# Kernel tuning notes

Hardware: AMD Instinct MI355X
Metric: run time of the kernel (lower is better)

The kernel has to match this reference:

```python
import jax, jax.numpy as jnp
import numpy as np

B, S, F_IN = 64, 168, 10
D, H, L = 512, 8, 4
HID, F_OUT, N_FUT = 2048, 1, 48
EPS = 1e-9


def _pos_encoding(d, position=168):
    pos = np.arange(position)[:, None].astype(np.float32)
    i = np.arange(d)[None, :].astype(np.float32)
    angle = pos / np.power(10000.0, 2.0 * (np.floor(i / 2.0)) / np.float32(d))
    angle[:, 0::2] = np.sin(angle[:, 0::2])
    angle[:, 1::2] = np.cos(angle[:, 1::2])
    return jnp.asarray(angle[None, ...], dtype=jnp.float32)  # [1, position, d]


def setup_inputs() -> dict:
    key = jax.random.key(0)
    ks = iter(jax.random.split(key, 64))
    s = 0.02

    def w(shape):
        return (jax.random.normal(next(ks), shape, jnp.float32) * s)

    inp = {
        "x": jax.random.normal(next(ks), (B, S, F_IN), jnp.float32),
        "mask": jnp.triu(jnp.ones((S, S), jnp.float32), k=1)[None, None],  # [1,1,S,S]
        "in_w": w((F_IN, D)), "in_b": jnp.zeros((D,), jnp.float32),
        "wq_w": w((L, D, D * H)), "wq_b": jnp.zeros((L, D * H), jnp.float32),
        "wk_w": w((L, D, D * H)), "wk_b": jnp.zeros((L, D * H), jnp.float32),
        "wv_w": w((L, D, D * H)), "wv_b": jnp.zeros((L, D * H), jnp.float32),
        "dn_w": w((L, D * H, D)), "dn_b": jnp.zeros((L, D), jnp.float32),
        "mh_w": w((L, D, HID)), "mh_b": jnp.zeros((L, HID), jnp.float32),
        "mo_w": w((L, HID, D)), "mo_b": jnp.zeros((L, D), jnp.float32),
        "ln1_g": jnp.ones((L, D), jnp.float32), "ln1_b": jnp.zeros((L, D), jnp.float32),
        "ln3_g": jnp.ones((L, D), jnp.float32), "ln3_b": jnp.zeros((L, D), jnp.float32),
        "out_w": w((D, F_OUT)), "out_b": jnp.zeros((F_OUT,), jnp.float32),
    }
    return inp


def _ln(h, g, b):
    m = jnp.mean(h, axis=-1, keepdims=True)
    v = jnp.mean((h - m) ** 2, axis=-1, keepdims=True)
    return (h - m) * jax.lax.rsqrt(v + EPS) * g + b


def _split(t):  # [B,S,H*D] -> [B,H,S,D]
    return t.reshape(B, S, H, D).transpose(0, 2, 1, 3)


def reference(x, mask, in_w, in_b, wq_w, wq_b, wk_w, wk_b, wv_w, wv_b,
              dn_w, dn_b, mh_w, mh_b, mo_w, mo_b,
              ln1_g, ln1_b, ln3_g, ln3_b, out_w, out_b):
    pe = _pos_encoding(D)  # [1,168,D]
    h = x @ in_w + in_b
    h = h * jnp.sqrt(jnp.float32(D)) + pe[:, :S, :]
    inv_sqrt_d = 1.0 / jnp.sqrt(jnp.float32(D))
    for i in range(L):
        q = _split(h @ wq_w[i] + wq_b[i])
        k = _split(h @ wk_w[i] + wk_b[i])
        v = _split(h @ wv_w[i] + wv_b[i])
        scores = jnp.einsum('bhqd,bhkd->bhqk', q, k) * inv_sqrt_d
        scores = scores + mask * (-1e9)
        attn_w = jax.nn.softmax(scores, axis=-1)
        att = jnp.einsum('bhqk,bhkd->bhqd', attn_w, v)
        att = att.transpose(0, 2, 1, 3).reshape(B, S, H * D)
        att = att @ dn_w[i] + dn_b[i]
        h1 = _ln(att + h, ln1_g[i], ln1_b[i])
        mlp = jax.nn.relu(h1 @ mh_w[i] + mh_b[i]) @ mo_w[i] + mo_b[i]
        h = _ln(mlp + h1, ln3_g[i], ln3_b[i])
    out = h @ out_w + out_b
    return out[:, -N_FUT:, :]
```

## Files before the change

kernel.cpp:

```cpp
#include <hip/hip_runtime.h>
#include <hip/hip_bf16.h>

typedef __bf16 bf16;
typedef __bf16 bf16x8 __attribute__((ext_vector_type(8)));
typedef __bf16 bf16x4v __attribute__((ext_vector_type(4)));
typedef float f32x4 __attribute__((ext_vector_type(4)));

#define MODE_BIAS 1
#define MODE_RELU 2
#define MODE_BF16 4
#define MODE_F32  8
#define MODE_RES  16
#define MODE_RESB 32
#define MODE_QKV  128
#define MODE_ATOMIC 256

__device__ __forceinline__ void stage16(const bf16* g, bf16* l)
{
  __builtin_amdgcn_global_load_lds(
      (const __attribute__((address_space(1))) void*)g,
      (__attribute__((address_space(3))) void*)l, 16, 0, 0);
}

__global__ __launch_bounds__(256) void gemm2(
    const bf16* __restrict__ A, const bf16* __restrict__ B,
    float* __restrict__ Cf, bf16* __restrict__ Cb,
    const float* __restrict__ bias, const float* __restrict__ resf,
    const bf16* __restrict__ resb,
    int N, int K, int lda, int ldb, int ldc, long qstride, int mode)
{
  __shared__ __attribute__((aligned(16))) bf16 smem[16384];
  bf16* sA = smem;
  bf16* sB = smem + 8192;

  int tid  = threadIdx.x;
  int lane = tid & 63;
  int wave = tid >> 6;
  int wm = (wave >> 1) * 64;
  int wn = (wave & 1) * 64;

  int nwg = gridDim.x * gridDim.y;
  int i0  = blockIdx.y * gridDim.x + blockIdx.x;
  int q   = nwg >> 3, r = nwg & 7;
  int xcd = i0 & 7, jj = i0 >> 3;
  int lid = (xcd < r ? xcd * (q + 1) : r * (q + 1) + (xcd - r) * q) + jj;
  int bx = lid % gridDim.x;
  int by = lid / gridDim.x;
  int bm0 = bx * 128;
  int bn0 = by * 128;
  long ks = (long)blockIdx.z * K;

  f32x4 acc[4][4];
  #pragma unroll
  for (int i = 0; i < 4; ++i)
    #pragma unroll
    for (int j = 0; j < 4; ++j)
      #pragma unroll
      for (int rr = 0; rr < 4; ++rr) acc[i][j][rr] = 0.f;

  int seg0 = wave, seg1 = wave + 4;
  int csw = ((lane & 3) ^ ((lane >> 3) & 3)) * 16;
  int r0s = seg0 * 16 + (lane >> 2);
  int r1s = seg1 * 16 + (lane >> 2);
  int rx = ((lane >> 4) ^ ((lane >> 1) & 3)) * 8;

  const char* gA0 = (const char*)A + ((long)(bm0 + r0s) * lda + ks) * 2 + csw;
  const char* gA1 = (const char*)A + ((long)(bm0 + r1s) * lda + ks) * 2 + csw;
  const char* gB0 = (const char*)B + ((long)(bn0 + r0s) * ldb + ks) * 2 + csw;
  const char* gB1 = (const char*)B + ((long)(bn0 + r1s) * ldb + ks) * 2 + csw;

  int nt = K >> 5;

  stage16((const bf16*)gA0, sA + seg0 * 512);
  stage16((const bf16*)gA1, sA + seg1 * 512);
  stage16((const bf16*)gB0, sB + seg0 * 512);
  stage16((const bf16*)gB1, sB + seg1 * 512);

  for (int t = 0; t < nt; ++t) {
    int p = t & 1;
    if (t + 1 < nt) {
      long ob = (long)(t + 1) * 64;
      int so = (p ^ 1) * 4096;
      stage16((const bf16*)(gA0 + ob), sA + so + seg0 * 512);
      stage16((const bf16*)(gA1 + ob), sA + so + seg1 * 512);
      stage16((const bf16*)(gB0 + ob), sB + so + seg0 * 512);
      stage16((const bf16*)(gB1 + ob), sB + so + seg1 * 512);
      asm volatile("s_waitcnt vmcnt(4)" ::: "memory");
    } else {
      asm volatile("s_waitcnt vmcnt(0)" ::: "memory");
    }
    asm volatile("s_barrier" ::: "memory");
    __builtin_amdgcn_sched_barrier(0);
    int po = p * 4096;
    bf16x8 aF[4], bF[4];
    #pragma unroll
    for (int i = 0; i < 4; ++i)
      aF[i] = *(const bf16x8*)(&sA[po + (wm + i * 16 + (lane & 15)) * 32 + rx]);
    #pragma unroll
    for (int j = 0; j < 4; ++j)
      bF[j] = *(const bf16x8*)(&sB[po + (wn + j * 16 + (lane & 15)) * 32 + rx]);
    __builtin_amdgcn_s_setprio(1);
    #pragma unroll
    for (int i = 0; i < 4; ++i)
      #pragma unroll
      for (int j = 0; j < 4; ++j)
        acc[i][j] = __builtin_amdgcn_mfma_f32_16x16x32_bf16(aF[i], bF[j], acc[i][j], 0, 0, 0);
    __builtin_amdgcn_s_setprio(0);
    asm volatile("s_waitcnt lgkmcnt(0)" ::: "memory");
    __builtin_amdgcn_sched_barrier(0);
    asm volatile("s_barrier" ::: "memory");
  }

  int lg = lane >> 4;
  int r0 = lg * 4;
  int cc = lane & 15;

  if (mode & MODE_ATOMIC) {
    #pragma unroll
    for (int j = 0; j < 4; ++j) {
      int gn = bn0 + wn + j * 16 + cc;
      #pragma unroll
      for (int i = 0; i < 4; ++i)
        #pragma unroll
        for (int rr = 0; rr < 4; ++rr) {
          int gm = bm0 + wm + i * 16 + r0 + rr;
          unsafeAtomicAdd(&Cf[(long)gm * ldc + gn], acc[i][j][rr]);
        }
    }
    return;
  }

  if ((mode & MODE_QKV) && bn0 >= 8192) {
    bf16* sS = smem;
    int nn0 = bn0 - 8192;
    #pragma unroll
    for (int ph = 0; ph < 2; ++ph) {
      if ((wn >> 6) == ph) {
        #pragma unroll
        for (int j = 0; j < 4; ++j) {
          int nl = j * 16 + cc;
          float bv = bias[bn0 + wn + j * 16 + cc];
          #pragma unroll
          for (int i = 0; i < 4; ++i)
            #pragma unroll
            for (int rr = 0; rr < 4; ++rr) {
              int m = wm + i * 16 + r0 + rr;
              sS[nl * 130 + m] = (bf16)(acc[i][j][rr] + bv);
            }
        }
      }
      __syncthreads();
      #pragma unroll
      for (int u = 0; u < 16; ++u) {
        int nrow = u * 4 + wave;
        int d = nn0 + ph * 64 + nrow;
        int hh = d >> 9, dd = d & 511;
        unsigned int pv = *(const unsigned int*)&sS[nrow * 130 + lane * 2];
        int m0 = bm0 + 2 * lane;
        int bl = m0 / 168;
        int s  = m0 - bl * 168;
        *(unsigned int*)&Cb[2 * qstride + ((long)(bl * 8 + hh) * 512 + dd) * 168 + s] = pv;
      }
      __syncthreads();
    }
    return;
  }

  if (mode & (MODE_QKV | MODE_BF16)) {
    bf16* sS = smem;
    long base;
    int ldx;
    if (mode & MODE_QKV) {
      int part = bn0 >> 12;
      base = (long)part * qstride + (bn0 & 4095);
      ldx = 4096;
    } else {
      base = (long)bn0;
      ldx = ldc;
    }
    #pragma unroll
    for (int ph = 0; ph < 2; ++ph) {
      if ((wm >> 6) == ph) {
        #pragma unroll
        for (int j = 0; j < 4; ++j) {
          float bv = (mode & MODE_BIAS) ? bias[bn0 + wn + j * 16 + cc] : 0.f;
          #pragma unroll
          for (int i = 0; i < 4; ++i) {
            #pragma unroll
            for (int rr = 0; rr < 4; ++rr) {
              float v = acc[i][j][rr] + bv;
              if (mode & MODE_RELU) v = fmaxf(v, 0.f);
              sS[(i * 16 + r0 + rr) * 136 + wn + j * 16 + cc] = (bf16)v;
            }
          }
        }
      }
      __syncthreads();
      #pragma unroll
      for (int it = 0; it < 4; ++it) {
        int idx = it * 256 + tid;
        int row = idx >> 4, seg = idx & 15;
        bf16x8 v = *(const bf16x8*)&sS[row * 136 + seg * 8];
        *(bf16x8*)&Cb[base + (long)(bm0 + ph * 64 + row) * ldx + seg * 8] = v;
      }
      __syncthreads();
    }
    return;
  }

  #pragma unroll
  for (int j = 0; j < 4; ++j) {
    int gn = bn0 + wn + j * 16 + cc;
    float bv = (mode & MODE_BIAS) ? bias[gn] : 0.f;
    #pragma unroll
    for (int i = 0; i < 4; ++i) {
      #pragma unroll
      for (int rr = 0; rr < 4; ++rr) {
        int gm = bm0 + wm + i * 16 + r0 + rr;
        float v = acc[i][j][rr] + bv;
        if (mode & MODE_RES)  v += resf[(long)gm * ldc + gn];
        if (mode & MODE_RESB) v += (float)resb[(long)gm * ldc + gn];
        if (mode & MODE_RELU) v = fmaxf(v, 0.f);
        if (mode & MODE_F32) {
          Cf[(long)gm * ldc + gn] = v;
        } else {
          Cb[(long)gm * ldc + gn] = (bf16)v;
        }
      }
    }
  }
}

__global__ __launch_bounds__(256) void init_acc(
    float* __restrict__ Xf, const float* __restrict__ srcF,
    const bf16* __restrict__ srcB, const float* __restrict__ bias, long n)
{
  long i = ((long)blockIdx.x * 256 + threadIdx.x) * 4;
  if (i >= n) return;
  int d = (int)(i & 511);
  float4 bv = *(const float4*)&bias[d];
  float4 v;
  if (srcF) {
    v = *(const float4*)&srcF[i];
  } else {
    bf16x4v s = *(const bf16x4v*)&srcB[i];
    v.x = (float)s[0]; v.y = (float)s[1]; v.z = (float)s[2]; v.w = (float)s[3];
  }
  v.x += bv.x; v.y += bv.y; v.z += bv.z; v.w += bv.w;
  *(float4*)&Xf[i] = v;
}

__global__ __launch_bounds__(256) void attn_fused(
    const bf16* __restrict__ Q, const bf16* __restrict__ K,
    const bf16* __restrict__ Vt, bf16* __restrict__ O)
{
  __shared__ __attribute__((aligned(16))) bf16 sQ[2 * 64 * 32];
  __shared__ __attribute__((aligned(16))) bf16 sK[2 * 192 * 32];
  __shared__ __attribute__((aligned(16))) bf16 sP[64 * 200];
  __shared__ __attribute__((aligned(16))) bf16 sV[256 * 32];

  int mt = blockIdx.x;
  int bh = blockIdx.y;
  int bl = bh >> 3, h = bh & 7;
  int tid = threadIdx.x, lane = tid & 63, wave = tid >> 6;

  const bf16* Qb = Q + ((long)bl * 168 + mt * 64) * 4096 + h * 512;
  const bf16* Kb = K + (long)bl * 168 * 4096 + h * 512;
  const bf16* Vb = Vt + (long)bh * 512 * 168;

  #pragma unroll
  for (int idx = tid; idx < 64 * 16; idx += 256) {
    int rr = idx >> 4;
    sP[rr * 200 + 176 + (idx & 15)] = (bf16)0.f;
  }

  int srw = wave * 16 + (lane >> 2);
  int scb = ((lane & 3) ^ ((lane >> 3) & 3)) * 16;
  int rx  = ((lane >> 4) ^ ((lane >> 1) & 3)) * 8;

  const char* gQ = (const char*)Qb + (long)srw * 8192 + scb;
  const char* gK = (const char*)Kb + (long)srw * 8192 + scb;

  f32x4 sacc[11];
  #pragma unroll
  for (int j = 0; j < 11; ++j)
    #pragma unroll
    for (int rr = 0; rr < 4; ++rr) sacc[j][rr] = 0.f;

  stage16((const bf16*)gQ, &sQ[wave * 512]);
  stage16((const bf16*)gK, &sK[wave * 512]);
  stage16((const bf16*)(gK + 64 * 8192), &sK[(wave + 4) * 512]);
  stage16((const bf16*)(gK + 128 * 8192), &sK[(wave + 8) * 512]);

  for (int t = 0; t < 16; ++t) {
    int p = t & 1;
    if (t < 15) {
      long ob = (long)(t + 1) * 64;
      int bq = (p ^ 1) * 2048, bk = (p ^ 1) * 6144;
      stage16((const bf16*)(gQ + ob), &sQ[bq + wave * 512]);
      stage16((const bf16*)(gK + ob), &sK[bk + wave * 512]);
      stage16((const bf16*)(gK + 64 * 8192 + ob), &sK[bk + (wave + 4) * 512]);
      stage16((const bf16*)(gK + 128 * 8192 + ob), &sK[bk + (wave + 8) * 512]);
      asm volatile("s_waitcnt vmcnt(4)" ::: "memory");
    } else {
      asm volatile("s_waitcnt vmcnt(0)" ::: "memory");
    }
    asm volatile("s_barrier" ::: "memory");
    __builtin_amdgcn_sched_barrier(0);
    bf16x8 aF = *(const bf16x8*)(&sQ[p * 2048 + (wave * 16 + (lane & 15)) * 32 + rx]);
    __builtin_amdgcn_s_setprio(1);
    #pragma unroll
    for (int j = 0; j < 11; ++j) {
      bf16x8 bF = *(const bf16x8*)(&sK[p * 6144 + (j * 16 + (lane & 15)) * 32 + rx]);
      sacc[j] = __builtin_amdgcn_mfma_f32_16x16x32_bf16(aF, bF, sacc[j], 0, 0, 0);
    }
    __builtin_amdgcn_s_setprio(0);
    asm volatile("s_waitcnt lgkmcnt(0)" ::: "memory");
    __builtin_amdgcn_sched_barrier(0);
    asm volatile("s_barrier" ::: "memory");
  }

  int rbase = wave * 16 + ((lane >> 4) << 2);
  #pragma unroll
  for (int rr = 0; rr < 4; ++rr) {
    int srow = mt * 64 + rbase + rr;
    float mx = -1e30f;
    #pragma unroll
    for (int j = 0; j < 11; ++j) {
      int col = j * 16 + (lane & 15);
      float v = sacc[j][rr] * 0.04419417382415922f;
      v = (col <= srow) ? v : -1e9f;
      sacc[j][rr] = v;
      mx = fmaxf(mx, v);
    }
    #pragma unroll
    for (int off = 1; off < 16; off <<= 1) mx = fmaxf(mx, __shfl_xor(mx, off, 16));
    float sum = 0.f;
    #pragma unroll
    for (int j = 0; j < 11; ++j) {
      float e = __expf(sacc[j][rr] - mx);
      sacc[j][rr] = e;
      sum += e;
    }
    #pragma unroll
    for (int off = 1; off < 16; off <<= 1) sum += __shfl_xor(sum, off, 16);
    float inv = 1.f / sum;
    #pragma unroll
    for (int j = 0; j < 11; ++j)
      sP[(rbase + rr) * 200 + j * 16 + (lane & 15)] = (bf16)(sacc[j][rr] * inv);
  }

  const char* gV = (const char*)Vb + (long)srw * 336 + scb;
  #pragma unroll 1
  for (int nc = 0; nc < 2; ++nc) {
    f32x4 oacc[16];
    #pragma unroll
    for (int t = 0; t < 16; ++t)
      #pragma unroll
      for (int rr = 0; rr < 4; ++rr) oacc[t][rr] = 0.f;

    for (int k0 = 0; k0 < 192; k0 += 32) {
      #pragma unroll
      for (int u = 0; u < 4; ++u)
        stage16((const bf16*)(gV + (long)(nc * 256 + u * 64) * 336 + (long)k0 * 2),
                &sV[(wave + u * 4) * 512]);
      __syncthreads();
      bf16x8 aF = *(const bf16x8*)(&sP[(wave * 16 + (lane & 15)) * 200 + k0 + (lane >> 4) * 8]);
      __builtin_amdgcn_s_setprio(1);
      #pragma unroll
      for (int t = 0; t < 16; ++t) {
        bf16x8 bF = *(const bf16x8*)(&sV[(t * 16 + (lane & 15)) * 32 + rx]);
        oacc[t] = __builtin_amdgcn_mfma_f32_16x16x32_bf16(aF, bF, oacc[t], 0, 0, 0);
      }
      __builtin_amdgcn_s_setprio(0);
      __syncthreads();
    }
    #pragma unroll
    for (int t = 0; t < 16; ++t) {
      int d = nc * 256 + t * 16 + (lane & 15);
      #pragma unroll
      for (int rr = 0; rr < 4; ++rr) {
        int srow = mt * 64 + rbase + rr;
        if (srow < 168)
          O[((long)bl * 168 + srow) * 4096 + h * 512 + d] = (bf16)oacc[t][rr];
      }
    }
  }
}

__global__ __launch_bounds__(256) void transpose_w(const float* __restrict__ in,
                                                   bf16* __restrict__ out,
                                                   int K, int N, long ostride, long obase)
{
  long zi = (long)blockIdx.z * K * N;
  long zo = (long)blockIdx.z * ostride + obase;
  __shared__ float t[32][33];
  int tx = threadIdx.x & 31;
  int ty = threadIdx.x >> 5;
  int n0 = blockIdx.x * 32;
  int k0 = blockIdx.y * 32;
  #pragma unroll
  for (int r = 0; r < 4; ++r) {
    int k = k0 + ty + r * 8, n = n0 + tx;
    if (k < K && n < N) t[ty + r * 8][tx] = in[zi + (long)k * N + n];
  }
  __syncthreads();
  #pragma unroll
  for (int r = 0; r < 4; ++r) {
    int n = n0 + ty + r * 8, k = k0 + tx;
    if (n < N && k < K) out[zo + (long)n * K + k] = (bf16)t[tx][ty + r * 8];
  }
}

__global__ __launch_bounds__(256) void merge_bias(const float* __restrict__ q,
                                                  const float* __restrict__ k,
                                                  const float* __restrict__ v,
                                                  float* __restrict__ o)
{
  int idx = blockIdx.x * 256 + threadIdx.x;
  if (idx >= 4 * 12288) return;
  int l = idx / 12288, r = idx - l * 12288;
  int part = r >> 12, n = r & 4095;
  const float* s = (part == 0) ? q : (part == 1) ? k : v;
  o[idx] = s[l * 4096 + n];
}

__global__ __launch_bounds__(256) void input_proj(const float* __restrict__ x,
                                                  const float* __restrict__ w,
                                                  const float* __restrict__ b,
                                                  float* __restrict__ hf,
                                                  bf16* __restrict__ hb)
{
  long idx = (long)blockIdx.x * 256 + threadIdx.x;
  long row = idx >> 9;
  int d = (int)(idx & 511);
  float acc = b[d];
  const float* xr = x + row * 10;
  #pragma unroll
  for (int f = 0; f < 10; ++f) acc += xr[f] * w[f * 512 + d];
  int s = (int)(row % 168);
  float rate = __expf(-(float)(d & ~1) * (9.210340371976184f / 512.f));
  float ang = (float)s * rate;
  float pe = (d & 1) ? cosf(ang) : sinf(ang);
  float v = acc * 22.627416997969522f + pe;
  hf[idx] = v;
  hb[idx] = (bf16)v;
}

__device__ __forceinline__ float block_sum256(float v, float* red)
{
  #pragma unroll
  for (int o = 32; o > 0; o >>= 1) v += __shfl_xor(v, o, 64);
  if ((threadIdx.x & 63) == 0) red[threadIdx.x >> 6] = v;
  __syncthreads();
  float tot = red[0] + red[1] + red[2] + red[3];
  __syncthreads();
  return tot;
}

__global__ __launch_bounds__(256) void ln_kernel(const float* __restrict__ X,
                                                 const float* __restrict__ g,
                                                 const float* __restrict__ bta,
                                                 float* __restrict__ Yf,
                                                 bf16* __restrict__ Yb)
{
  __shared__ float red[4];
  long row = blockIdx.x;
  int t = threadIdx.x;
  const float* x = X + row * 512;
  float v0 = x[t], v1 = x[t + 256];
  float mean = block_sum256(v0 + v1, red) * (1.f / 512.f);
  float d0 = v0 - mean, d1 = v1 - mean;
  float var = block_sum256(d0 * d0 + d1 * d1, red) * (1.f / 512.f);
  float rs = rsqrtf(var + 1e-9f);
  float y0 = d0 * rs * g[t] + bta[t];
  float y1 = d1 * rs * g[t + 256] + bta[t + 256];
  if (Yf) {
    Yf[row * 512 + t] = y0;
    Yf[row * 512 + t + 256] = y1;
  }
  Yb[row * 512 + t] = (bf16)y0;
  Yb[row * 512 + t + 256] = (bf16)y1;
}

__global__ __launch_bounds__(256) void out_proj(const float* __restrict__ hf,
                                                const float* __restrict__ ow,
                                                const float* __restrict__ ob,
                                                float* __restrict__ out)
{
  int gid = blockIdx.x * 256 + threadIdx.x;
  int wid = gid >> 6;
  int lane = gid & 63;
  if (wid >= 64 * 48) return;
  int b = wid / 48, j = wid - b * 48;
  long row = (long)b * 168 + 120 + j;
  const float* x = hf + row * 512;
  float s = 0.f;
  #pragma unroll
  for (int t = 0; t < 8; ++t) s += x[lane + t * 64] * ow[lane + t * 64];
  #pragma unroll
  for (int o = 32; o > 0; o >>= 1) s += __shfl_xor(s, o, 64);
  if (lane == 0) out[wid] = s + ob[0];
}

extern "C" void kernel_launch(void* const* d_in, const int* in_sizes, int n_in,
                              void* d_out, int out_size, void* d_ws, size_t ws_size,
                              hipStream_t stream)
{
  const float* x     = (const float*)d_in[0];
  const float* in_w  = (const float*)d_in[2];
  const float* in_b  = (const float*)d_in[3];
  const float* wq_w  = (const float*)d_in[4];
  const float* wq_b  = (const float*)d_in[5];
  const float* wk_w  = (const float*)d_in[6];
  const float* wk_b  = (const float*)d_in[7];
  const float* wv_w  = (const float*)d_in[8];
  const float* wv_b  = (const float*)d_in[9];
  const float* dn_w  = (const float*)d_in[10];
  const float* dn_b  = (const float*)d_in[11];
  const float* mh_w  = (const float*)d_in[12];
  const float* mh_b  = (const float*)d_in[13];
  const float* mo_w  = (const float*)d_in[14];
  const float* mo_b  = (const float*)d_in[15];
  const float* ln1_g = (const float*)d_in[16];
  const float* ln1_b = (const float*)d_in[17];
  const float* ln3_g = (const float*)d_in[18];
  const float* ln3_b = (const float*)d_in[19];
  const float* out_w = (const float*)d_in[20];
  const float* out_b = (const float*)d_in[21];
  float* out = (float*)d_out;

  auto al = [](size_t b) { return (b + 255) & ~(size_t)255; };
  size_t off = 0;
  auto alloc = [&](size_t bytes) -> char* {
    char* p = (char*)d_ws + off;
    off += al(bytes);
    return p;
  };

  bf16*  wqkvT = (bf16*)alloc(4L * 12288 * 512 * 2);
  float* qkvB  = (float*)alloc(4L * 12288 * 4);
  bf16*  dnT   = (bf16*)alloc(4L * 512 * 4096 * 2);
  bf16*  mhT   = (bf16*)alloc(4L * 2048 * 512 * 2);
  bf16*  moT   = (bf16*)alloc(4L * 512 * 2048 * 2);
  float* hF    = (float*)alloc(10752L * 512 * 4);
  bf16*  hB    = (bf16*)alloc(10752L * 512 * 2);
  float* Xf    = (float*)alloc(10752L * 512 * 4);

  const int  CB = 16, NC = 4;
  const long Mc = (long)CB * 168;
  const long qstride = Mc * 4096;
  bf16* Qc = (bf16*)alloc((size_t)(3 * qstride) * 2);
  bf16* Kc  = Qc + qstride;
  bf16* Vtc = Qc + 2 * qstride;
  bf16* h1b = Qc;
  bf16* m1c = Qc + 10752L * 512;

  transpose_w<<<dim3(128, 16, 4), 256, 0, stream>>>(wq_w, wqkvT, 512, 4096, 12288L * 512, 0);
  transpose_w<<<dim3(128, 16, 4), 256, 0, stream>>>(wk_w, wqkvT, 512, 4096, 12288L * 512, 4096L * 512);
  transpose_w<<<dim3(128, 16, 4), 256, 0, stream>>>(wv_w, wqkvT, 512, 4096, 12288L * 512, 8192L * 512);
  transpose_w<<<dim3(16, 128, 4), 256, 0, stream>>>(dn_w, dnT, 4096, 512, 512L * 4096, 0);
  transpose_w<<<dim3(64, 16, 4), 256, 0, stream>>>(mh_w, mhT, 512, 2048, 2048L * 512, 0);
  transpose_w<<<dim3(16, 64, 4), 256, 0, stream>>>(mo_w, moT, 2048, 512, 512L * 2048, 0);
  merge_bias<<<(4 * 12288 + 255) / 256, 256, 0, stream>>>(wq_b, wk_b, wv_b, qkvB);

  input_proj<<<10752 * 512 / 256, 256, 0, stream>>>(x, in_w, in_b, hF, hB);

  const int cM = (int)(Mc / 128);

  for (int l = 0; l < 4; ++l) {
    for (int c = 0; c < NC; ++c) {
      long row0 = (long)c * Mc;

      gemm2<<<dim3(cM, 96), 256, 0, stream>>>(
          hB + row0 * 512, wqkvT + (long)l * 12288 * 512, nullptr, Qc,
          qkvB + (long)l * 12288, nullptr, nullptr,
          12288, 512, 512, 512, 0, qstride, MODE_BIAS | MODE_QKV);

      attn_fused<<<dim3(3, CB * 8), 256, 0, stream>>>(Qc, Kc, Vtc, Qc);

      init_acc<<<(int)(Mc * 512 / 1024), 256, 0, stream>>>(
          Xf + row0 * 512, hF + row0 * 512, nullptr, dn_b + (long)l * 512, Mc * 512);
      gemm2<<<dim3(cM, 4, 8), 256, 0, stream>>>(
          Qc, dnT + (long)l * 512 * 4096, Xf + row0 * 512, nullptr,
          nullptr, nullptr, nullptr,
          512, 512, 4096, 4096, 512, 0, MODE_ATOMIC);
    }

    ln_kernel<<<10752, 256, 0, stream>>>(Xf, ln1_g + l * 512, ln1_b + l * 512,
                                         nullptr, h1b);

    gemm2<<<dim3(84, 16), 256, 0, stream>>>(
        h1b, mhT + (long)l * 2048 * 512, nullptr, m1c,
        mh_b + (long)l * 2048, nullptr, nullptr,
        2048, 512, 512, 512, 2048, 0, MODE_BIAS | MODE_RELU | MODE_BF16);

    init_acc<<<10752 * 512 / 1024, 256, 0, stream>>>(
        Xf, nullptr, h1b, mo_b + (long)l * 512, 10752L * 512);
    gemm2<<<dim3(84, 4, 4), 256, 0, stream>>>(
        m1c, moT + (long)l * 512 * 2048, Xf, nullptr,
        nullptr, nullptr, nullptr,
        512, 512, 2048, 2048, 512, 0, MODE_ATOMIC);

    ln_kernel<<<10752, 256, 0, stream>>>(Xf, ln3_g + l * 512, ln3_b + l * 512,
                                         hF, hB);
  }

  out_proj<<<(64 * 48 * 64) / 256, 256, 0, stream>>>(hF, out_w, out_b, out);
}
```

Baseline: 3.239 ms.

## Replace atomic split-K accumulation with partial buffers and fused epilogue

Measured after the change: 2.721 ms. 16.0% less time.

```diff
diff --git a/kernel.cpp b/kernel.cpp
--- a/kernel.cpp
+++ b/kernel.cpp
@@ -13,7 +13,7 @@
 #define MODE_RES  16
 #define MODE_RESB 32
 #define MODE_QKV  128
-#define MODE_ATOMIC 256
+#define MODE_PART 256
 
 __device__ __forceinline__ void stage16(const bf16* g, bf16* l)
 {
@@ -115,7 +115,8 @@
   int r0 = lg * 4;
   int cc = lane & 15;
 
-  if (mode & MODE_ATOMIC) {
+  if (mode & MODE_PART) {
+    float* Cfz = Cf + (long)blockIdx.z * qstride;
     #pragma unroll
     for (int j = 0; j < 4; ++j) {
       int gn = bn0 + wn + j * 16 + cc;
@@ -124,7 +125,7 @@
         #pragma unroll
         for (int rr = 0; rr < 4; ++rr) {
           int gm = bm0 + wm + i * 16 + r0 + rr;
-          unsafeAtomicAdd(&Cf[(long)gm * ldc + gn], acc[i][j][rr]);
+          Cfz[(long)gm * ldc + gn] = acc[i][j][rr];
         }
     }
     return;
@@ -231,22 +232,22 @@
   }
 }
 
-__global__ __launch_bounds__(256) void init_acc(
-    float* __restrict__ Xf, const float* __restrict__ srcF,
-    const bf16* __restrict__ srcB, const float* __restrict__ bias, long n)
+__global__ __launch_bounds__(256) void dn_reduce(
+    float* __restrict__ Xf, const float* __restrict__ P,
+    const float* __restrict__ hF, const float* __restrict__ bias,
+    long n, long pstride)
 {
   long i = ((long)blockIdx.x * 256 + threadIdx.x) * 4;
   if (i >= n) return;
   int d = (int)(i & 511);
+  float4 v  = *(const float4*)&hF[i];
   float4 bv = *(const float4*)&bias[d];
-  float4 v;
-  if (srcF) {
-    v = *(const float4*)&srcF[i];
-  } else {
-    bf16x4v s = *(const bf16x4v*)&srcB[i];
-    v.x = (float)s[0]; v.y = (float)s[1]; v.z = (float)s[2]; v.w = (float)s[3];
-  }
   v.x += bv.x; v.y += bv.y; v.z += bv.z; v.w += bv.w;
+  #pragma unroll
+  for (int z = 0; z < 4; ++z) {
+    float4 p = *(const float4*)&P[(long)z * pstride + i];
+    v.x += p.x; v.y += p.y; v.z += p.z; v.w += p.w;
+  }
   *(float4*)&Xf[i] = v;
 }
 
@@ -555,6 +556,8 @@
   bf16* Vtc = Qc + 2 * qstride;
   bf16* h1b = Qc;
   bf16* m1c = Qc + 10752L * 512;
+  float* dnP = (float*)Kc;
+  const long pstride = Mc * 512;
 
   transpose_w<<<dim3(128, 16, 4), 256, 0, stream>>>(wq_w, wqkvT, 512, 4096, 12288L * 512, 0);
   transpose_w<<<dim3(128, 16, 4), 256, 0, stream>>>(wk_w, wqkvT, 512, 4096, 12288L * 512, 4096L * 512);
@@ -579,12 +582,13 @@
 
       attn_fused<<<dim3(3, CB * 8), 256, 0, stream>>>(Qc, Kc, Vtc, Qc);
 
-      init_acc<<<(int)(Mc * 512 / 1024), 256, 0, stream>>>(
-          Xf + row0 * 512, hF + row0 * 512, nullptr, dn_b + (long)l * 512, Mc * 512);
-      gemm2<<<dim3(cM, 4, 8), 256, 0, stream>>>(
-          Qc, dnT + (long)l * 512 * 4096, Xf + row0 * 512, nullptr,
+      gemm2<<<dim3(cM, 4, 4), 256, 0, stream>>>(
+          Qc, dnT + (long)l * 512 * 4096, dnP, nullptr,
           nullptr, nullptr, nullptr,
-          512, 512, 4096, 4096, 512, 0, MODE_ATOMIC);
+          512, 1024, 4096, 4096, 512, pstride, MODE_PART);
+      dn_reduce<<<(int)(Mc * 512 / 1024), 256, 0, stream>>>(
+          Xf + row0 * 512, dnP, hF + row0 * 512, dn_b + (long)l * 512,
+          Mc * 512, pstride);
     }
 
     ln_kernel<<<10752, 256, 0, stream>>>(Xf, ln1_g + l * 512, ln1_b + l * 512,
@@ -595,12 +599,10 @@
         mh_b + (long)l * 2048, nullptr, nullptr,
         2048, 512, 512, 512, 2048, 0, MODE_BIAS | MODE_RELU | MODE_BF16);
 
-    init_acc<<<10752 * 512 / 1024, 256, 0, stream>>>(
-        Xf, nullptr, h1b, mo_b + (long)l * 512, 10752L * 512);
-    gemm2<<<dim3(84, 4, 4), 256, 0, stream>>>(
+    gemm2<<<dim3(84, 4), 256, 0, stream>>>(
         m1c, moT + (long)l * 512 * 2048, Xf, nullptr,
-        nullptr, nullptr, nullptr,
-        512, 512, 2048, 2048, 512, 0, MODE_ATOMIC);
+        mo_b + (long)l * 512, nullptr, h1b,
+        512, 2048, 2048, 2048, 512, 0, MODE_BIAS | MODE_RESB | MODE_F32);
 
     ln_kernel<<<10752, 256, 0, stream>>>(Xf, ln3_g + l * 512, ln3_b + l * 512,
                                          hF, hB);
```
